# Optimization experiments

Measured on AMD Instinct MI355X. Metric: run time of the kernel, lower is better.

Reference implementation:

```python
import jax, jax.numpy as jnp
import numpy as np

DIM = 4096
N_HEADS = 32
N_KV_HEADS = 8
HEAD_DIM = DIM // N_HEADS            # 128
GROUP = N_HEADS // N_KV_HEADS        # 4 heads share each kv head


def setup_inputs() -> dict:
    key = jax.random.key(0)
    k1, k2, k3, k4 = jax.random.split(key, 4)
    B, S = 2, 2048
    x = jax.random.normal(k1, (B, S, DIM), dtype=jnp.float32)
    # nn.Linear weights are [out_features, in_features]
    Wq = jax.random.normal(k2, (N_HEADS * HEAD_DIM, DIM), dtype=jnp.float32) * 0.02
    Wkv = jax.random.normal(k3, (2 * N_KV_HEADS * HEAD_DIM, DIM), dtype=jnp.float32) * 0.02
    Wo = jax.random.normal(k4, (DIM, N_HEADS * HEAD_DIM), dtype=jnp.float32) * 0.02
    return {"x": x, "Wq": Wq, "Wkv": Wkv, "Wo": Wo, "start_pos": 0}


def reference(x, Wq, Wkv, Wo, start_pos):
    B, S, _ = x.shape
    total_len = start_pos + S
    # projections (Linear: x @ W.T)
    q = (x @ Wq.T).reshape(B, S, N_HEADS, HEAD_DIM)                  # (B,S,H,D)
    kv = (x @ Wkv.T).reshape(B, S, 2 * N_KV_HEADS, HEAD_DIM)
    k, v = jnp.split(kv, 2, axis=2)                                   # (B,S,Hkv,D) each
    # cache write + read with start_pos=0 is identity on k, v (prefill)
    # inflate kv heads: repeat_interleave along head axis
    k = jnp.repeat(k, GROUP, axis=2)                                  # (B,T,H,D)
    v = jnp.repeat(v, GROUP, axis=2)
    scale = HEAD_DIM ** -0.5
    scores = jnp.einsum('bqhd,bkhd->bhqk', q, k) * scale              # (B,H,S,T)
    q_idx = jnp.arange(total_len - S, total_len)[:, None]
    k_idx = jnp.arange(total_len)[None, :]
    causal = q_idx >= k_idx                                           # (S,T)
    scores = jnp.where(causal[None, None], scores, -jnp.inf)
    probs = jax.nn.softmax(scores, axis=-1)
    attn = jnp.einsum('bhqk,bkhd->bqhd', probs, v)                    # (B,S,H,D)
    attn = attn.reshape(B, S, N_HEADS * HEAD_DIM)
    return attn @ Wo.T                                                # (B,S,dim)
```

## Files before the change

kernel.cpp:

```cpp
#include <hip/hip_runtime.h>

typedef __bf16 bf16x8 __attribute__((ext_vector_type(8)));
typedef __bf16 bf16x4 __attribute__((ext_vector_type(4)));
typedef float f32x4 __attribute__((ext_vector_type(4)));
typedef unsigned short u16;
typedef unsigned short u16x8 __attribute__((ext_vector_type(8)));

#define DIM 4096
#define NHEADS 32
#define NKV 8
#define HD 128
#define BB 2
#define SS 2048
#define MROWS (BB*SS)
#define QKVP 6144
#define QSCALE 0.08838834764831843f

#define WAIT_LGKM0 asm volatile("s_waitcnt lgkmcnt(0)" ::: "memory")
#define WAIT_VM0   asm volatile("s_waitcnt vmcnt(0)" ::: "memory")
#define SGB0       __builtin_amdgcn_sched_barrier(0)

__device__ __forceinline__ u16 f2bf(float f) {
  unsigned int u = __float_as_uint(f);
  u += 0x7fffu + ((u >> 16) & 1u);
  return (u16)(u >> 16);
}

__device__ __forceinline__ void gload16(const void* g, void* l) {
  __builtin_amdgcn_global_load_lds(
      (const __attribute__((address_space(1))) unsigned int*)g,
      (__attribute__((address_space(3))) unsigned int*)l, 16, 0, 0);
}

__device__ __forceinline__ bf16x4 tr16(const void* p) {
  bf16x4 d;
  asm volatile("ds_read_b64_tr_b16 %0, %1"
               : "=v"(d)
               : "v"((const __attribute__((address_space(3))) u16*)p)
               : "memory");
  return d;
}

template<int CTRL>
__device__ __forceinline__ float dpp_ror(float x) {
  return __int_as_float(__builtin_amdgcn_update_dpp(
      0, __float_as_int(x), CTRL, 0xF, 0xF, false));
}
__device__ __forceinline__ float red16_max(float v) {
  v = fmaxf(v, dpp_ror<0x121>(v));
  v = fmaxf(v, dpp_ror<0x122>(v));
  v = fmaxf(v, dpp_ror<0x124>(v));
  v = fmaxf(v, dpp_ror<0x128>(v));
  return v;
}
__device__ __forceinline__ float red16_sum(float v) {
  v += dpp_ror<0x121>(v);
  v += dpp_ror<0x122>(v);
  v += dpp_ror<0x124>(v);
  v += dpp_ror<0x128>(v);
  return v;
}

__global__ __launch_bounds__(256) void f2b_kernel(const float* __restrict__ in,
                                                  u16* __restrict__ out, int n8) {
  int i = blockIdx.x * 256 + threadIdx.x;
  if (i >= n8) return;
  const float4* in4 = (const float4*)in;
  float4 a = in4[2*(size_t)i];
  float4 b = in4[2*(size_t)i + 1];
  u16x8 o;
  o[0]=f2bf(a.x); o[1]=f2bf(a.y); o[2]=f2bf(a.z); o[3]=f2bf(a.w);
  o[4]=f2bf(b.x); o[5]=f2bf(b.y); o[6]=f2bf(b.z); o[7]=f2bf(b.w);
  ((u16x8*)out)[i] = o;
}

template<int OUTF32>
__global__ __launch_bounds__(512, 2) void gemm256(
    const u16* __restrict__ A, const u16* __restrict__ Bm, void* __restrict__ C,
    int M, int N, int K, int nbx, int acut, float a0, float a1) {
  __shared__ char smem[131072];
  char* smA = smem;
  char* smB = smem + 65536;

  const int t = threadIdx.x;
  const int l = t & 63, w = t >> 6;
  const int l15 = l & 15, l4 = l >> 4;
  const int wm = w >> 2, wn = w & 3;

  const int nwg = gridDim.x;
  const int cpx = nwg >> 3;
  const int sw = (blockIdx.x & 7) * cpx + (blockIdx.x >> 3);
  const int bx = sw % nbx, by = sw / nbx;
  const int row0 = by * 256, col0 = bx * 256;
  const float alpha = (col0 < acut) ? a0 : a1;

  f32x4 acc[8][4] = {};

  auto stage = [&](int k0, int pb) {
    char* Ad = smA + pb * 32768;
    char* Bd = smB + pb * 32768;
    #pragma unroll
    for (int i = 0; i < 4; ++i) {
      int o = i*8192 + w*1024 + l*16;
      int row = o >> 7;
      int sc = ((o >> 4) & 7) ^ (row & 7);
      gload16((const char*)A + ((size_t)(row0 + row)*K + k0)*2 + sc*16,
              Ad + i*8192 + w*1024);
      gload16((const char*)Bm + ((size_t)(col0 + row)*K + k0)*2 + sc*16,
              Bd + i*8192 + w*1024);
    }
  };

  const int ntiles = K >> 6;
  stage(0, 0);
  WAIT_VM0;
  __builtin_amdgcn_s_barrier();

  for (int kt = 0; kt < ntiles; ++kt) {
    const char* Ab = smA + (kt & 1) * 32768;
    const char* Bb = smB + (kt & 1) * 32768;
    if (kt + 1 < ntiles) stage((kt + 1) << 6, (kt + 1) & 1);

    #pragma unroll
    for (int q = 0; q < 4; ++q) {
      const int qm = q >> 1, qn = q & 1;
      bf16x8 af[4][2], bfv[2][2];
      #pragma unroll
      for (int mi = 0; mi < 4; ++mi)
        #pragma unroll
        for (int kk = 0; kk < 2; ++kk) {
          int row = wm*128 + (qm*4 + mi)*16 + l15;
          int sc = (kk*4 + l4) ^ (row & 7);
          af[mi][kk] = *(const bf16x8*)(Ab + row*128 + sc*16);
        }
      #pragma unroll
      for (int ni = 0; ni < 2; ++ni)
        #pragma unroll
        for (int kk = 0; kk < 2; ++kk) {
          int row = wn*64 + (qn*2 + ni)*16 + l15;
          int sc = (kk*4 + l4) ^ (row & 7);
          bfv[ni][kk] = *(const bf16x8*)(Bb + row*128 + sc*16);
        }
      __builtin_amdgcn_s_setprio(1);
      #pragma unroll
      for (int kk = 0; kk < 2; ++kk)
        #pragma unroll
        for (int mi = 0; mi < 4; ++mi)
          #pragma unroll
          for (int ni = 0; ni < 2; ++ni)
            acc[qm*4 + mi][qn*2 + ni] = __builtin_amdgcn_mfma_f32_16x16x32_bf16(
                af[mi][kk], bfv[ni][kk], acc[qm*4 + mi][qn*2 + ni], 0, 0, 0);
      __builtin_amdgcn_s_setprio(0);
      __builtin_amdgcn_s_barrier();
    }
    WAIT_VM0;
    __builtin_amdgcn_s_barrier();
  }

  #pragma unroll
  for (int mi = 0; mi < 8; ++mi) {
    #pragma unroll
    for (int ni = 0; ni < 4; ++ni) {
      #pragma unroll
      for (int r = 0; r < 4; ++r) {
        size_t rr = (size_t)(row0 + wm*128 + mi*16 + l4*4 + r);
        size_t cc = (size_t)(col0 + wn*64 + ni*16 + l15);
        float v = acc[mi][ni][r] * alpha;
        if (OUTF32) ((float*)C)[rr*(size_t)N + cc] = v;
        else        ((u16*)C)[rr*(size_t)N + cc] = f2bf(v);
      }
    }
  }
}

__global__ __launch_bounds__(256, 2) void attn_kernel(
    const u16* __restrict__ QKV,
    u16* __restrict__ O) {
  __shared__ u16 Ks[2][64*128];
  __shared__ u16 Vs[2][64*128];
  __shared__ u16 Ps[4][1024];
  const int t = threadIdx.x;
  const int l = t & 63, w = t >> 6;
  const int l15 = l & 15, l4 = l >> 4;
  const int pair = blockIdx.x, h = blockIdx.y, b = blockIdx.z;
  const int hkv = h >> 2;
  const u16* Kg = QKV + (size_t)(b*SS) * QKVP + DIM + hkv*HD;
  const u16* Vg = Kg + NKV*HD;
  u16* Pw = &Ps[w][0];

  auto stage = [&](u16* Ksb, u16* Vsb, int kv0) {
    const u16* Kr = Kg + (size_t)kv0 * QKVP;
    const u16* Vr = Vg + (size_t)kv0 * QKVP;
    #pragma unroll
    for (int i = 0; i < 4; ++i) {
      int o = i*4096 + w*1024 + l*16;
      int row = o >> 8;
      int sc = l15 ^ (row & 7);
      gload16((const char*)(Kr + (size_t)row * QKVP) + sc*16,
              (char*)Ksb + i*4096 + w*1024);
    }
    #pragma unroll
    for (int i = 0; i < 4; ++i) {
      int cb = i*4 + w;
      int kv = cb*4 + ((l & 7) >> 1);
      int d0 = ((l >> 3) << 4) + (l & 1)*8;
      gload16((const char*)(Vr + (size_t)kv * QKVP + d0),
              (char*)Vsb + cb*1024);
    }
  };

  for (int half = 0; half < 2; ++half) {
    const int qb = half ? (15 - pair) : pair;
    const int q0 = qb * 128;
    const int q0w = q0 + w*32;

    const size_t qbase = ((size_t)(b*SS + q0w)) * QKVP + h*HD;
    bf16x8 qf[2][4];
    #pragma unroll
    for (int m = 0; m < 2; ++m)
      #pragma unroll
      for (int kd = 0; kd < 4; ++kd)
        qf[m][kd] = *(const bf16x8*)&QKV[qbase + (size_t)(m*16 + l15)*QKVP + kd*32 + l4*8];

    f32x4 oacc[2][8] = {};
    float mrun[2][4], lrun[2][4];
    #pragma unroll
    for (int m = 0; m < 2; ++m)
      #pragma unroll
      for (int r = 0; r < 4; ++r) { mrun[m][r] = -1e30f; lrun[m][r] = 0.f; }

    const int nst = 2*qb + 2;
    stage(Ks[0], Vs[0], 0);
    WAIT_VM0;
    __builtin_amdgcn_s_barrier();
    SGB0;

    for (int st = 0; st < nst; ++st) {
      const int kv0 = st * 64;
      u16* Ksb = Ks[st & 1];
      u16* Vsb = Vs[st & 1];
      if (st + 1 < nst) stage(Ks[(st+1) & 1], Vs[(st+1) & 1], kv0 + 64);

      if (kv0 <= q0w + 31) {
        f32x4 sacc[2][4] = {};
        __builtin_amdgcn_s_setprio(1);
        #pragma unroll
        for (int kd = 0; kd < 4; ++kd) {
          bf16x8 kf[4];
          #pragma unroll
          for (int n = 0; n < 4; ++n) {
            int row = n*16 + l15;
            int off = (row << 8) | (((kd*4 + l4) ^ (row & 7)) << 4);
            kf[n] = *(const bf16x8*)((const char*)Ksb + off);
          }
          #pragma unroll
          for (int m = 0; m < 2; ++m)
            #pragma unroll
            for (int n = 0; n < 4; ++n)
              sacc[m][n] = __builtin_amdgcn_mfma_f32_16x16x32_bf16(qf[m][kd], kf[n], sacc[m][n], 0, 0, 0);
        }
        __builtin_amdgcn_s_setprio(0);

        if (st >= 2*qb) {
          #pragma unroll
          for (int n = 0; n < 4; ++n) {
            int ki = kv0 + n*16 + l15;
            #pragma unroll
            for (int m = 0; m < 2; ++m)
              #pragma unroll
              for (int r = 0; r < 4; ++r) {
                int qi = q0w + m*16 + l4*4 + r;
                if (ki > qi) sacc[m][n][r] = -1e30f;
              }
          }
        }

        float pr[2][4][4];
        #pragma unroll
        for (int m = 0; m < 2; ++m) {
          #pragma unroll
          for (int r = 0; r < 4; ++r) {
            float s0 = sacc[m][0][r], s1 = sacc[m][1][r];
            float s2 = sacc[m][2][r], s3 = sacc[m][3][r];
            float vm = fmaxf(fmaxf(s0, s1), fmaxf(s2, s3));
            vm = red16_max(vm);
            float mo = mrun[m][r];
            float mnew = fmaxf(mo, vm);
            float al = __expf(mo - mnew);
            float p0 = __expf(s0 - mnew), p1 = __expf(s1 - mnew);
            float p2 = __expf(s2 - mnew), p3 = __expf(s3 - mnew);
            float rs = red16_sum((p0 + p1) + (p2 + p3));
            mrun[m][r] = mnew;
            lrun[m][r] = lrun[m][r]*al + rs;
            #pragma unroll
            for (int dn = 0; dn < 8; ++dn) oacc[m][dn][r] *= al;
            pr[m][r][0] = p0; pr[m][r][1] = p1; pr[m][r][2] = p2; pr[m][r][3] = p3;
          }
        }

        #pragma unroll
        for (int kvh = 0; kvh < 2; ++kvh) {
          #pragma unroll
          for (int m = 0; m < 2; ++m)
            #pragma unroll
            for (int nn = 0; nn < 2; ++nn) {
              int n = kvh*2 + nn;
              bf16x4 w4;
              w4[0] = (__bf16)pr[m][0][n]; w4[1] = (__bf16)pr[m][1][n];
              w4[2] = (__bf16)pr[m][2][n]; w4[3] = (__bf16)pr[m][3][n];
              *(bf16x4*)((char*)Pw + ((nn*4 + (l15 >> 2))*2 + m)*128
                                   + (l15 & 3)*32 + l4*8) = w4;
            }
          const char* pb = (const char*)Pw + l4*512 + l15*8;
          bf16x4 a00 = tr16(pb);
          bf16x4 a01 = tr16(pb + 256);
          bf16x4 a10 = tr16(pb + 128);
          bf16x4 a11 = tr16(pb + 384);
          const char* vb = (const char*)Vsb + l4*2048 + l15*8 + kvh*8192;
          bf16x4 b0[8], b1[8];
          #pragma unroll
          for (int dn = 0; dn < 8; ++dn) {
            b0[dn] = tr16(vb + dn*128);
            b1[dn] = tr16(vb + dn*128 + 1024);
          }
          WAIT_LGKM0; SGB0;
          bf16x8 pa0 = __builtin_shufflevector(a00, a01, 0,1,2,3,4,5,6,7);
          bf16x8 pa1 = __builtin_shufflevector(a10, a11, 0,1,2,3,4,5,6,7);
          __builtin_amdgcn_s_setprio(1);
          #pragma unroll
          for (int dn = 0; dn < 8; ++dn) {
            bf16x8 v8 = __builtin_shufflevector(b0[dn], b1[dn], 0,1,2,3,4,5,6,7);
            oacc[0][dn] = __builtin_amdgcn_mfma_f32_16x16x32_bf16(pa0, v8, oacc[0][dn], 0, 0, 0);
            oacc[1][dn] = __builtin_amdgcn_mfma_f32_16x16x32_bf16(pa1, v8, oacc[1][dn], 0, 0, 0);
          }
          __builtin_amdgcn_s_setprio(0);
        }
      }

      WAIT_VM0;
      __builtin_amdgcn_s_barrier();
      SGB0;
    }

    const size_t obase = ((size_t)(b*SS + q0w)) * DIM + h*HD;
    #pragma unroll
    for (int m = 0; m < 2; ++m) {
      #pragma unroll
      for (int r = 0; r < 4; ++r) {
        float inv = 1.0f / lrun[m][r];
        int srow = m*16 + l4*4 + r;
        #pragma unroll
        for (int dn = 0; dn < 8; ++dn)
          O[obase + (size_t)srow*DIM + dn*16 + l15] = f2bf(oacc[m][dn][r] * inv);
      }
    }
  }
}

extern "C" void kernel_launch(void* const* d_in, const int* in_sizes, int n_in,
                              void* d_out, int out_size, void* d_ws, size_t ws_size,
                              hipStream_t stream) {
  const float* x   = (const float*)d_in[0];
  const float* Wq  = (const float*)d_in[1];
  const float* Wkv = (const float*)d_in[2];
  const float* Wo  = (const float*)d_in[3];

  if (ws_size < (160ull << 20)) return;
  char* ws = (char*)d_ws;
  u16* xb   = (u16*)(ws);
  u16* Wqb  = (u16*)(ws + (32ull  << 20));
  u16* Wkvb = (u16*)(ws + (64ull  << 20));
  u16* Wob  = (u16*)(ws + (80ull  << 20));
  u16* QKVb = (u16*)(ws + (112ull << 20));
  u16* attnb = xb;

  f2b_kernel<<<8192, 256, 0, stream>>>(x,   xb,   2097152);
  f2b_kernel<<<8192, 256, 0, stream>>>(Wq,  Wqb,  2097152);
  f2b_kernel<<<4096, 256, 0, stream>>>(Wkv, Wkvb, 1048576);
  f2b_kernel<<<8192, 256, 0, stream>>>(Wo,  Wob,  2097152);

  gemm256<0><<<dim3(16*24), 512, 0, stream>>>(xb, Wqb, QKVb,
                                              MROWS, QKVP, DIM, 24, DIM, QSCALE, 1.0f);

  attn_kernel<<<dim3(8, NHEADS, BB), 256, 0, stream>>>(QKVb, attnb);

  gemm256<1><<<dim3(16*16), 512, 0, stream>>>(attnb, Wob, d_out,
                                              MROWS, DIM, DIM, 16, 0, 1.0f, 1.0f);
}
```

Before: 568.5 us.

## Use four-stage K=32 LDS pipeline with three tiles in flight in gemm256

Replaces the double-buffered K=64 tile pipeline with a 4-buffer ring of K=32 tiles, prefetching three tiles ahead and waiting with partial vmcnt counts instead of draining all loads. The LDS layout is re-swizzled so two rows share a 128-byte line, and each iteration reads all A/B fragments once before issuing 32 MFMAs. The aim is to hide global load latency better and cut per-iteration barriers. In exchange it takes twice as many loop iterations with smaller MFMA batches, and correctness depends on the vmcnt accounting matching the loads issued per stage.

```diff
diff --git a/kernel.cpp b/kernel.cpp
--- a/kernel.cpp
+++ b/kernel.cpp
@@ -18,6 +18,8 @@
 
 #define WAIT_LGKM0 asm volatile("s_waitcnt lgkmcnt(0)" ::: "memory")
 #define WAIT_VM0   asm volatile("s_waitcnt vmcnt(0)" ::: "memory")
+#define WAIT_VM4   asm volatile("s_waitcnt vmcnt(4)" ::: "memory")
+#define WAIT_VM8   asm volatile("s_waitcnt vmcnt(8)" ::: "memory")
 #define SGB0       __builtin_amdgcn_sched_barrier(0)
 
 __device__ __forceinline__ u16 f2bf(float f) {
@@ -79,8 +81,6 @@
     const u16* __restrict__ A, const u16* __restrict__ Bm, void* __restrict__ C,
     int M, int N, int K, int nbx, int acut, float a0, float a1) {
   __shared__ char smem[131072];
-  char* smA = smem;
-  char* smB = smem + 65536;
 
   const int t = threadIdx.x;
   const int l = t & 63, w = t >> 6;
@@ -96,65 +96,66 @@
 
   f32x4 acc[8][4] = {};
 
-  auto stage = [&](int k0, int pb) {
-    char* Ad = smA + pb * 32768;
-    char* Bd = smB + pb * 32768;
-    #pragma unroll
-    for (int i = 0; i < 4; ++i) {
-      int o = i*8192 + w*1024 + l*16;
-      int row = o >> 7;
-      int sc = ((o >> 4) & 7) ^ (row & 7);
-      gload16((const char*)A + ((size_t)(row0 + row)*K + k0)*2 + sc*16,
-              Ad + i*8192 + w*1024);
-      gload16((const char*)Bm + ((size_t)(col0 + row)*K + k0)*2 + sc*16,
-              Bd + i*8192 + w*1024);
+  auto stage = [&](int kt) {
+    const int bsel = kt & 3;
+    const int k0 = kt << 5;
+    char* Ad = smem + bsel * 16384;
+    char* Bd = smem + 65536 + bsel * 16384;
+    #pragma unroll
+    for (int i = 0; i < 2; ++i) {
+      int o = (i*8 + w)*64 + l;
+      int j = o >> 3;
+      int cs = (o & 7) ^ (j & 7);
+      int r = 2*j + (cs >> 2);
+      int kc = (cs & 3) * 8;
+      gload16((const char*)A + ((size_t)(row0 + r)*K + k0 + kc)*2,
+              Ad + (i*8 + w)*1024);
+      gload16((const char*)Bm + ((size_t)(col0 + r)*K + k0 + kc)*2,
+              Bd + (i*8 + w)*1024);
     }
   };
 
-  const int ntiles = K >> 6;
-  stage(0, 0);
-  WAIT_VM0;
+  const int nt = K >> 5;
+  stage(0); stage(1); stage(2);
+  WAIT_VM8;
   __builtin_amdgcn_s_barrier();
-
-  for (int kt = 0; kt < ntiles; ++kt) {
-    const char* Ab = smA + (kt & 1) * 32768;
-    const char* Bb = smB + (kt & 1) * 32768;
-    if (kt + 1 < ntiles) stage((kt + 1) << 6, (kt + 1) & 1);
-
-    #pragma unroll
-    for (int q = 0; q < 4; ++q) {
-      const int qm = q >> 1, qn = q & 1;
-      bf16x8 af[4][2], bfv[2][2];
-      #pragma unroll
-      for (int mi = 0; mi < 4; ++mi)
-        #pragma unroll
-        for (int kk = 0; kk < 2; ++kk) {
-          int row = wm*128 + (qm*4 + mi)*16 + l15;
-          int sc = (kk*4 + l4) ^ (row & 7);
-          af[mi][kk] = *(const bf16x8*)(Ab + row*128 + sc*16);
-        }
-      #pragma unroll
-      for (int ni = 0; ni < 2; ++ni)
-        #pragma unroll
-        for (int kk = 0; kk < 2; ++kk) {
-          int row = wn*64 + (qn*2 + ni)*16 + l15;
-          int sc = (kk*4 + l4) ^ (row & 7);
-          bfv[ni][kk] = *(const bf16x8*)(Bb + row*128 + sc*16);
-        }
-      __builtin_amdgcn_s_setprio(1);
-      #pragma unroll
-      for (int kk = 0; kk < 2; ++kk)
-        #pragma unroll
-        for (int mi = 0; mi < 4; ++mi)
-          #pragma unroll
-          for (int ni = 0; ni < 2; ++ni)
-            acc[qm*4 + mi][qn*2 + ni] = __builtin_amdgcn_mfma_f32_16x16x32_bf16(
-                af[mi][kk], bfv[ni][kk], acc[qm*4 + mi][qn*2 + ni], 0, 0, 0);
-      __builtin_amdgcn_s_setprio(0);
-      __builtin_amdgcn_s_barrier();
-    }
-    WAIT_VM0;
+  SGB0;
+
+  for (int kt = 0; kt < nt; ++kt) {
+    if (kt + 3 < nt) { stage(kt + 3); WAIT_VM8; }
+    else if (kt + 2 < nt) { WAIT_VM4; }
+    else if (kt + 1 < nt) { WAIT_VM0; }
     __builtin_amdgcn_s_barrier();
+    SGB0;
+
+    const char* Ab = smem + (kt & 3) * 16384;
+    const char* Bb = smem + 65536 + (kt & 3) * 16384;
+    bf16x8 af[8], bfv[4];
+    #pragma unroll
+    for (int mi = 0; mi < 8; ++mi) {
+      int r = wm*128 + mi*16 + l15;
+      int j = r >> 1;
+      int c = ((r & 1)*4 + l4) ^ (j & 7);
+      af[mi] = *(const bf16x8*)(Ab + j*128 + c*16);
+    }
+    #pragma unroll
+    for (int ni = 0; ni < 4; ++ni) {
+      int r = wn*64 + ni*16 + l15;
+      int j = r >> 1;
+      int c = ((r & 1)*4 + l4) ^ (j & 7);
+      bfv[ni] = *(const bf16x8*)(Bb + j*128 + c*16);
+    }
+    __builtin_amdgcn_s_setprio(1);
+    #pragma unroll
+    for (int mi = 0; mi < 8; ++mi)
+      #pragma unroll
+      for (int ni = 0; ni < 4; ++ni)
+        acc[mi][ni] = __builtin_amdgcn_mfma_f32_16x16x32_bf16(
+            af[mi], bfv[ni], acc[mi][ni], 0, 0, 0);
+    __builtin_amdgcn_s_setprio(0);
+    SGB0;
+    __builtin_amdgcn_s_barrier();
+    SGB0;
   }
 
   #pragma unroll
```

Result: no change. 571.4 us (+0.5%).

## Restructure GEMM main loop into finely interleaved load/compute phases and fuse conversions

Applied to the files above, without the earlier changes.

The bf16 GEMM main loop is rewritten as an 8-phase software pipeline. Each phase issues part of the next tile's global-to-LDS loads, reads LDS fragments into registers that are reused across quadrants, and runs a block of MFMAs, with partial vmcnt waits in place of full drains. The goal is to overlap global memory traffic with matrix-core work and cut LDS re-reads. Separately, the four fp32-to-bf16 conversion launches are merged into one kernel to remove launch overhead. The trade-off is many more barriers and a tighter dependency on the exact wait counts being correct.

```diff
diff --git a/kernel.cpp b/kernel.cpp
--- a/kernel.cpp
+++ b/kernel.cpp
@@ -18,6 +18,7 @@
 
 #define WAIT_LGKM0 asm volatile("s_waitcnt lgkmcnt(0)" ::: "memory")
 #define WAIT_VM0   asm volatile("s_waitcnt vmcnt(0)" ::: "memory")
+#define WAIT_VM4   asm volatile("s_waitcnt vmcnt(4)" ::: "memory")
 #define SGB0       __builtin_amdgcn_sched_barrier(0)
 
 __device__ __forceinline__ u16 f2bf(float f) {
@@ -61,17 +62,24 @@
   return v;
 }
 
-__global__ __launch_bounds__(256) void f2b_kernel(const float* __restrict__ in,
-                                                  u16* __restrict__ out, int n8) {
+__global__ __launch_bounds__(256) void f2b4_kernel(
+    const float* __restrict__ xa, const float* __restrict__ xb,
+    const float* __restrict__ xc, const float* __restrict__ xd,
+    u16* __restrict__ oa, u16* __restrict__ ob,
+    u16* __restrict__ oc, u16* __restrict__ od) {
   int i = blockIdx.x * 256 + threadIdx.x;
-  if (i >= n8) return;
+  const float* in; u16* out; int k;
+  if (i < 2097152)      { in = xa; out = oa; k = i; }
+  else if (i < 4194304) { in = xb; out = ob; k = i - 2097152; }
+  else if (i < 5242880) { in = xc; out = oc; k = i - 4194304; }
+  else                  { in = xd; out = od; k = i - 5242880; }
   const float4* in4 = (const float4*)in;
-  float4 a = in4[2*(size_t)i];
-  float4 b = in4[2*(size_t)i + 1];
+  float4 a = in4[2*(size_t)k];
+  float4 b = in4[2*(size_t)k + 1];
   u16x8 o;
   o[0]=f2bf(a.x); o[1]=f2bf(a.y); o[2]=f2bf(a.z); o[3]=f2bf(a.w);
   o[4]=f2bf(b.x); o[5]=f2bf(b.y); o[6]=f2bf(b.z); o[7]=f2bf(b.w);
-  ((u16x8*)out)[i] = o;
+  ((u16x8*)out)[k] = o;
 }
 
 template<int OUTF32>
@@ -79,8 +87,6 @@
     const u16* __restrict__ A, const u16* __restrict__ Bm, void* __restrict__ C,
     int M, int N, int K, int nbx, int acut, float a0, float a1) {
   __shared__ char smem[131072];
-  char* smA = smem;
-  char* smB = smem + 65536;
 
   const int t = threadIdx.x;
   const int l = t & 63, w = t >> 6;
@@ -96,65 +102,123 @@
 
   f32x4 acc[8][4] = {};
 
-  auto stage = [&](int k0, int pb) {
-    char* Ad = smA + pb * 32768;
-    char* Bd = smB + pb * 32768;
+  const int j1 = t >> 3;
+  const int cs1 = (t & 7) ^ (j1 & 7);
+  const u16* pA = A  + (size_t)(row0 + j1) * K + cs1 * 8;
+  const u16* pB = Bm + (size_t)(col0 + j1) * K + cs1 * 8;
+  const int nt = K >> 6;
+  const int ldst = w * 1024;
+
+  auto stA = [&](int tile, int h) {
+    if (tile >= nt) return;
+    const u16* s = pA + (size_t)(h * 128) * K + tile * 64;
+    char* dst = (char*)smem + (tile & 1) * 32768 + h * 16384 + ldst;
+    gload16(s, dst);
+    gload16(s + (size_t)64 * K, dst + 8192);
+  };
+  auto stB = [&](int tile, int h) {
+    if (tile >= nt) return;
+    const u16* s = pB + (size_t)(h * 128) * K + tile * 64;
+    char* dst = (char*)smem + 65536 + (tile & 1) * 32768 + h * 16384 + ldst;
+    gload16(s, dst);
+    gload16(s + (size_t)64 * K, dst + 8192);
+  };
+
+  const int cxk0 = ((0 * 4 + l4) ^ (l15 & 7)) * 16;
+  const int cxk1 = ((1 * 4 + l4) ^ (l15 & 7)) * 16;
+  const int abase = wm * 16384 + l15 * 128;
+  const int bbase = 65536 + (wn >> 1) * 16384 + (wn & 1) * 8192 + l15 * 128;
+
+  bf16x8 Ar[4][2], B0r[2][2], B1r[2][2];
+
+  auto rdA = [&](int d, int qm) {
+    const char* p = (const char*)smem + d * 32768 + qm * 8192 + abase;
     #pragma unroll
     for (int i = 0; i < 4; ++i) {
-      int o = i*8192 + w*1024 + l*16;
-      int row = o >> 7;
-      int sc = ((o >> 4) & 7) ^ (row & 7);
-      gload16((const char*)A + ((size_t)(row0 + row)*K + k0)*2 + sc*16,
-              Ad + i*8192 + w*1024);
-      gload16((const char*)Bm + ((size_t)(col0 + row)*K + k0)*2 + sc*16,
-              Bd + i*8192 + w*1024);
+      Ar[i][0] = *(const bf16x8*)(p + i * 2048 + cxk0);
+      Ar[i][1] = *(const bf16x8*)(p + i * 2048 + cxk1);
     }
   };
-
-  const int ntiles = K >> 6;
-  stage(0, 0);
-  WAIT_VM0;
-  __builtin_amdgcn_s_barrier();
-
-  for (int kt = 0; kt < ntiles; ++kt) {
-    const char* Ab = smA + (kt & 1) * 32768;
-    const char* Bb = smB + (kt & 1) * 32768;
-    if (kt + 1 < ntiles) stage((kt + 1) << 6, (kt + 1) & 1);
-
-    #pragma unroll
-    for (int q = 0; q < 4; ++q) {
-      const int qm = q >> 1, qn = q & 1;
-      bf16x8 af[4][2], bfv[2][2];
-      #pragma unroll
-      for (int mi = 0; mi < 4; ++mi)
-        #pragma unroll
-        for (int kk = 0; kk < 2; ++kk) {
-          int row = wm*128 + (qm*4 + mi)*16 + l15;
-          int sc = (kk*4 + l4) ^ (row & 7);
-          af[mi][kk] = *(const bf16x8*)(Ab + row*128 + sc*16);
-        }
-      #pragma unroll
-      for (int ni = 0; ni < 2; ++ni)
-        #pragma unroll
-        for (int kk = 0; kk < 2; ++kk) {
-          int row = wn*64 + (qn*2 + ni)*16 + l15;
-          int sc = (kk*4 + l4) ^ (row & 7);
-          bfv[ni][kk] = *(const bf16x8*)(Bb + row*128 + sc*16);
-        }
-      __builtin_amdgcn_s_setprio(1);
-      #pragma unroll
-      for (int kk = 0; kk < 2; ++kk)
-        #pragma unroll
-        for (int mi = 0; mi < 4; ++mi)
-          #pragma unroll
-          for (int ni = 0; ni < 2; ++ni)
-            acc[qm*4 + mi][qn*2 + ni] = __builtin_amdgcn_mfma_f32_16x16x32_bf16(
-                af[mi][kk], bfv[ni][kk], acc[qm*4 + mi][qn*2 + ni], 0, 0, 0);
-      __builtin_amdgcn_s_setprio(0);
-      __builtin_amdgcn_s_barrier();
-    }
-    WAIT_VM0;
-    __builtin_amdgcn_s_barrier();
+  auto rdB = [&](bf16x8 (&BR)[2][2], int d, int qn) {
+    const char* p = (const char*)smem + d * 32768 + qn * 4096 + bbase;
+    #pragma unroll
+    for (int n = 0; n < 2; ++n) {
+      BR[n][0] = *(const bf16x8*)(p + n * 2048 + cxk0);
+      BR[n][1] = *(const bf16x8*)(p + n * 2048 + cxk1);
+    }
+  };
+
+#define MM16(QM, QN, BR) \
+  do { \
+    __builtin_amdgcn_s_setprio(1); \
+    _Pragma("unroll") \
+    for (int i = 0; i < 4; ++i) \
+      _Pragma("unroll") \
+      for (int n = 0; n < 2; ++n) \
+        _Pragma("unroll") \
+        for (int kk = 0; kk < 2; ++kk) \
+          acc[(QM)*4 + i][(QN)*2 + n] = __builtin_amdgcn_mfma_f32_16x16x32_bf16( \
+              Ar[i][kk], BR[n][kk], acc[(QM)*4 + i][(QN)*2 + n], 0, 0, 0); \
+    __builtin_amdgcn_s_setprio(0); \
+  } while (0)
+
+#define PH_BAR  __builtin_amdgcn_s_barrier()
+
+  stB(0, 0); stB(0, 1); stA(0, 0); stA(0, 1); stB(1, 0); stB(1, 1);
+  WAIT_VM4;
+  PH_BAR;
+
+  const int niter = nt >> 1;
+  for (int j = 0; j < niter; ++j) {
+    const int tb = 2 * j + 1, tc = 2 * j + 2, td = 2 * j + 3;
+
+    rdA(0, 0); rdB(B0r, 0, 0); SGB0;
+    stA(tb, 0);
+    PH_BAR; WAIT_LGKM0; SGB0;
+    MM16(0, 0, B0r);
+    PH_BAR;
+
+    rdB(B1r, 0, 1); SGB0;
+    stA(tb, 1);
+    PH_BAR; WAIT_LGKM0; SGB0;
+    MM16(0, 1, B1r);
+    PH_BAR;
+
+    rdA(0, 1); SGB0;
+    stB(tc, 0);
+    PH_BAR; WAIT_LGKM0; SGB0;
+    MM16(1, 1, B1r);
+    PH_BAR;
+
+    stB(tc, 1);
+    PH_BAR;
+    MM16(1, 0, B0r);
+    if (tc < nt) { WAIT_VM4; } else { WAIT_VM0; }
+    PH_BAR;
+
+    rdA(1, 0); rdB(B0r, 1, 0); SGB0;
+    stA(tc, 0);
+    PH_BAR; WAIT_LGKM0; SGB0;
+    MM16(0, 0, B0r);
+    PH_BAR;
+
+    rdB(B1r, 1, 1); SGB0;
+    stA(tc, 1);
+    PH_BAR; WAIT_LGKM0; SGB0;
+    MM16(0, 1, B1r);
+    PH_BAR;
+
+    rdA(1, 1); SGB0;
+    stB(td, 0);
+    PH_BAR; WAIT_LGKM0; SGB0;
+    MM16(1, 1, B1r);
+    PH_BAR;
+
+    stB(td, 1);
+    PH_BAR;
+    MM16(1, 0, B0r);
+    if (td < nt) { WAIT_VM4; } else { WAIT_VM0; }
+    PH_BAR;
   }
 
   #pragma unroll
@@ -171,6 +235,8 @@
       }
     }
   }
+#undef MM16
+#undef PH_BAR
 }
 
 __global__ __launch_bounds__(256, 2) void attn_kernel(
@@ -374,10 +440,7 @@
   u16* QKVb = (u16*)(ws + (112ull << 20));
   u16* attnb = xb;
 
-  f2b_kernel<<<8192, 256, 0, stream>>>(x,   xb,   2097152);
-  f2b_kernel<<<8192, 256, 0, stream>>>(Wq,  Wqb,  2097152);
-  f2b_kernel<<<4096, 256, 0, stream>>>(Wkv, Wkvb, 1048576);
-  f2b_kernel<<<8192, 256, 0, stream>>>(Wo,  Wob,  2097152);
+  f2b4_kernel<<<28672, 256, 0, stream>>>(x, Wq, Wkv, Wo, xb, Wqb, Wkvb, Wob);
 
   gemm256<0><<<dim3(16*24), 512, 0, stream>>>(xb, Wqb, QKVb,
                                               MROWS, QKVP, DIM, 24, DIM, QSCALE, 1.0f);
```

Result: faster. 526.0 us (-7.5%).
